# Kernel optimization log

Measured on AMD Instinct MI355X. Metric: run time of the kernel, lower is better.

## Reference

```python
import jax, jax.numpy as jnp
import numpy as np
import math

D_MODEL = 512
KEY_DIM = 128
NUM_LAYERS = 2
TEMP = 30.0
NORM_EPS = 1e-5
NORM_SCALE = math.sqrt(1.0 / (D_MODEL * 4 * 4))


def _l2norm_lastdim(x):
    # F.normalize(x, p=2, dim=-1): x / max(||x||, 1e-12)
    n = jnp.sqrt(jnp.sum(x * x, axis=-1, keepdims=True))
    return x / jnp.maximum(n, 1e-12)


def _attn(q, k, v, WK, bK):
    # q: [Sq,B,D], k: [Sk,B,D], v: [Sk,B,D] -> [Sq,B,D]
    wq = _l2norm_lastdim(q @ WK + bK)            # [Sq,B,K]
    wk = _l2norm_lastdim(k @ WK + bK)            # [Sk,B,K]
    dot = jnp.einsum('qbk,sbk->bqs', wq, wk)     # cosine sims
    aff = jax.nn.softmax(dot * TEMP, axis=-1)
    return jnp.einsum('bqs,sbd->qbd', aff, v)


def _instance_norm(x, h, w):
    # x: [HW,B,D]; InstanceL2Norm over (D,h,w) per batch element, size_average=True
    HW, B, D = x.shape
    ss = jnp.sum(x * x, axis=(0, 2))             # [B]
    factor = NORM_SCALE * jnp.sqrt((D * h * w) / (ss + NORM_EPS))
    return x * factor[None, :, None]


def _encoder(src4d, WKs, bKs):
    B, D, H, W = src4d.shape
    x = src4d.reshape(B, D, H * W).transpose(2, 0, 1)   # [HW,B,D]
    for _ in range(NUM_LAYERS):
        x = _instance_norm(x + _attn(x, x, x, WKs, bKs), H, W)
    return x  # memory [HW,B,D]


def _decoder(tgt4d, memory, pos, WKs, bKs, WKc, bKc):
    B, D, H, W = tgt4d.shape
    x = tgt4d.reshape(B, D, H * W).transpose(2, 0, 1)   # [HW,B,D]
    for _ in range(NUM_LAYERS):
        x = _instance_norm(x + _attn(x, x, x, WKs, bKs), H, W)
        mask = _attn(x, memory, pos, WKc, bKc)
        t2 = _instance_norm(x * mask, H, W)
        t3 = _attn(x, memory, memory * pos, WKc, bKc)
        t4 = _instance_norm(x + t3, H, W)
        x = _instance_norm(t2 + t4, H, W)
    feat = x.reshape(H, W, B, D).transpose(2, 3, 0, 1)  # [B,D,H,W]
    return feat


def setup_inputs() -> dict:
    key = jax.random.key(0)
    k1, k2, k3, k4, k5 = jax.random.split(key, 5)
    B, D, H, W = 16, D_MODEL, 32, 32
    std = math.sqrt(2.0 / KEY_DIM)
    return {
        'train_feat': jax.random.normal(k1, (B, D, H, W), jnp.float32),
        'test_feat': jax.random.normal(k2, (B, D, H, W), jnp.float32),
        'train_label': jax.random.uniform(k3, (B, H, W), jnp.float32),
        'WK_self': jax.random.normal(k4, (D, KEY_DIM), jnp.float32) * std,
        'bK_self': jnp.zeros((KEY_DIM,), jnp.float32),
        'WK_cross': jax.random.normal(k5, (D, KEY_DIM), jnp.float32) * std,
        'bK_cross': jnp.zeros((KEY_DIM,), jnp.float32),
    }


def reference(train_feat, test_feat, train_label, WK_self, bK_self, WK_cross, bK_cross):
    B, D, H, W = train_feat.shape
    memory = _encoder(train_feat, WK_self, bK_self)              # [HW,B,D]
    # pos: label [B,H,W] -> [HW,B,1] -> broadcast to [HW,B,D]
    pos = jnp.broadcast_to(train_label.reshape(B, H * W).T[:, :, None], (H * W, B, D))
    encoded_feat = _decoder(train_feat, memory, pos, WK_self, bK_self, WK_cross, bK_cross)
    decoded_feat = _decoder(test_feat, memory, pos, WK_self, bK_self, WK_cross, bK_cross)
    return (encoded_feat, decoded_feat)
```

## Files before the change

kernel.cpp:

```cpp
#include <hip/hip_runtime.h>
#include <math.h>

#define NB 16
#define SEQ 1024
#define DM 512
#define KD 128
#define TEMP_F 30.0f
#define NS_F 0.011048543456039805f
#define DS_F 524288.0f

#define SS_IDX(grp, b) (((grp) * NB + (b)) * 16)
#define SS_STRIDE 768
#define SS_STAGES 12
#define SS_FLOATS (SS_STRIDE * SS_STAGES)

typedef short bf16x8 __attribute__((ext_vector_type(8)));
typedef float f32x4 __attribute__((ext_vector_type(4)));
typedef unsigned short us;
typedef unsigned short us8 __attribute__((ext_vector_type(8)));

__device__ __forceinline__ us f2bf(float x) {
    union { float f; unsigned u; } v; v.f = x;
    unsigned r = v.u + 0x7fffu + ((v.u >> 16) & 1u);
    return (us)(r >> 16);
}
__device__ __forceinline__ float bf2f(us h) {
    union { unsigned u; float f; } v; v.u = ((unsigned)h) << 16;
    return v.f;
}

#define GLL16(gp, lp) __builtin_amdgcn_global_load_lds( \
    (__attribute__((address_space(1))) void*)(unsigned long long)(gp), \
    (__attribute__((address_space(3))) void*)(unsigned)(unsigned long long)(lp), 16, 0, 0)

__global__ __launch_bounds__(256) void k_transpose_in(const float* __restrict__ src,
                                                      us* __restrict__ XC,
                                                      us* __restrict__ XT) {
    __shared__ float tile[32][33];
    const int b = blockIdx.z;
    const int d0 = blockIdx.x * 32;
    const int s0 = blockIdx.y * 32;
    const int tx = threadIdx.x, ty = threadIdx.y;
    const float* p = src + (size_t)b * DM * SEQ;
    us* pt = XT + (size_t)b * DM * SEQ;
    us* pc = XC + (size_t)b * SEQ * 1024;
#pragma unroll
    for (int j = 0; j < 32; j += 8) {
        const size_t o = (size_t)(d0 + ty + j) * SEQ + s0 + tx;
        const float v = p[o];
        tile[ty + j][tx] = v;
        pt[o] = f2bf(v);
    }
    __syncthreads();
#pragma unroll
    for (int j = 0; j < 4; ++j) {
        const int s = s0 + ty + j * 8;
        const int d = d0 + tx;
        const float v = tile[tx][ty + j * 8];
        const us h = f2bf(v);
        pc[(size_t)s * 1024 + d] = h;
        pc[(size_t)s * 1024 + 512 + d] = f2bf(v - bf2f(h));
    }
}

__global__ __launch_bounds__(256) void k_mklabel(const us* __restrict__ MT,
                                                 const float* __restrict__ label,
                                                 us* __restrict__ ML) {
    const int b = blockIdx.y;
    const size_t off = ((size_t)blockIdx.x * 256 + threadIdx.x) * 8;
    const int s = (int)(off & (SEQ - 1));
    const size_t o = (size_t)b * DM * SEQ + off;
    us8 v = *(const us8*)(MT + o);
    const float4 l0 = *(const float4*)(label + (size_t)b * SEQ + s);
    const float4 l1 = *(const float4*)(label + (size_t)b * SEQ + s + 4);
    us8 r;
    r[0] = f2bf(bf2f(v[0]) * l0.x); r[1] = f2bf(bf2f(v[1]) * l0.y);
    r[2] = f2bf(bf2f(v[2]) * l0.z); r[3] = f2bf(bf2f(v[3]) * l0.w);
    r[4] = f2bf(bf2f(v[4]) * l1.x); r[5] = f2bf(bf2f(v[5]) * l1.y);
    r[6] = f2bf(bf2f(v[6]) * l1.z); r[7] = f2bf(bf2f(v[7]) * l1.w);
    *(us8*)(ML + o) = r;
}

__global__ __launch_bounds__(256) void k_wsplit(const float* __restrict__ WK,
                                                us* __restrict__ WC) {
    const int k = blockIdx.x;
    for (int d = threadIdx.x; d < DM; d += 256) {
        const float v = WK[(size_t)d * KD + k];
        const us h = f2bf(v);
        WC[(size_t)k * 1024 + d] = h;
        WC[(size_t)k * 1024 + 512 + d] = f2bf(v - bf2f(h));
    }
}

__global__ __launch_bounds__(256) void k_proj(const us* __restrict__ XC,
                                              const us* __restrict__ WC,
                                              const float* __restrict__ bK,
                                              us* __restrict__ Wout) {
    const int row0 = blockIdx.x * 32;
    __shared__ short As[32 * 64], Bs[128 * 64];
    __shared__ float ssp[2][32];
    const int tid = threadIdx.x, w = tid >> 6, l = tid & 63;
    const int wm = (w >> 1) * 16, wn = (w & 1) * 64;
    const int sr = l >> 3, sc = (((l & 7) ^ (l >> 3)) << 3);
    const int lr = l & 15, lk = (l >> 4) * 8;
    const int sx = (lr & 7) << 3;
    f32x4 acc[4] = {};
    for (int k0 = 0; k0 < 1536; k0 += 64) {
        const int ak0 = (k0 < 1024) ? k0 : k0 - 1024;
        const int bk0 = (k0 < 512) ? k0 : k0 - 512;
        GLL16(XC + (size_t)(row0 + w * 8 + sr) * 1024 + ak0 + sc, &As[w * 512]);
#pragma unroll
        for (int cc = 0; cc < 4; ++cc) {
            const int c = 4 * w + cc;
            GLL16(WC + (size_t)(c * 8 + sr) * 1024 + bk0 + sc, &Bs[c * 512]);
        }
        __syncthreads();
#pragma unroll
        for (int kc = 0; kc < 2; ++kc) {
            const int kk = kc * 32 + lk;
            const bf16x8 a = *(const bf16x8*)&As[(wm + lr) * 64 + (kk ^ sx)];
            bf16x8 bb[4];
#pragma unroll
            for (int fn = 0; fn < 4; ++fn)
                bb[fn] = *(const bf16x8*)&Bs[(wn + fn * 16 + lr) * 64 + (kk ^ sx)];
#pragma unroll
            for (int fn = 0; fn < 4; ++fn)
                acc[fn] = __builtin_amdgcn_mfma_f32_16x16x32_bf16(a, bb[fn], acc[fn], 0, 0, 0);
        }
        __syncthreads();
    }
    const int er = l & 15, eq = (l >> 4) * 4;
    const int nh = w & 1;
    float bkv[4];
#pragma unroll
    for (int fn = 0; fn < 4; ++fn) bkv[fn] = bK[wn + fn * 16 + er];
    float vv[4][4];
#pragma unroll
    for (int r = 0; r < 4; ++r) {
        float ss = 0.f;
#pragma unroll
        for (int fn = 0; fn < 4; ++fn) {
            const float t = acc[fn][r] + bkv[fn];
            vv[fn][r] = t;
            ss += t * t;
        }
#pragma unroll
        for (int o = 8; o > 0; o >>= 1) ss += __shfl_xor(ss, o, 64);
        if (er == 0) ssp[nh][wm + eq + r] = ss;
    }
    __syncthreads();
#pragma unroll
    for (int r = 0; r < 4; ++r) {
        const int rowloc = wm + eq + r;
        const float tot = ssp[0][rowloc] + ssp[1][rowloc];
        const float invn = 1.0f / fmaxf(sqrtf(tot), 1e-12f);
        const size_t ro = (size_t)(row0 + rowloc) * 256;
#pragma unroll
        for (int fn = 0; fn < 4; ++fn) {
            const float ov = vv[fn][r] * invn;
            const us h = f2bf(ov);
            Wout[ro + wn + fn * 16 + er] = h;
            Wout[ro + 128 + wn + fn * 16 + er] = f2bf(ov - bf2f(h));
        }
    }
}

__global__ __launch_bounds__(512, 2) void k_attn(const us* __restrict__ Qc,
                                                 const us* __restrict__ Kc,
                                                 const us* __restrict__ VT,
                                                 const us* __restrict__ XC,
                                                 const float* __restrict__ labelp,
                                                 float* __restrict__ MVEC,
                                                 float* __restrict__ Cout,
                                                 float* __restrict__ SS, int mode) {
    const int b = blockIdx.x;
    const int q0 = blockIdx.y * 64;
    __shared__ short KL[2][4 * 32 * 64];
    __shared__ short VL[2][512 * 32];
    __shared__ us PL[64 * 40];
    __shared__ float RSL[2][64], RLL[2][64];
    __shared__ float INVL[64], MVL[64];
    __shared__ float LBL[1024];
    __shared__ float ps[3][8];
    const int tid = threadIdx.x, w = tid >> 6, l = tid & 63;
    const int lr = l & 15, g = l >> 4, lk = g * 8;
    const int qa = w & 3, sh = w >> 2;
    const int kx = (lr & 7) << 3;
    const us* Qb = Qc + (size_t)b * SEQ * 256;
    const us* Kb = Kc + (size_t)b * SEQ * 256;
    const us* Vb = VT + (size_t)b * DM * SEQ;

    const us* Qrow = Qb + (size_t)(q0 + qa * 16 + lr) * 256;
    bf16x8 qh[4], ql[4];
#pragma unroll
    for (int kc = 0; kc < 4; ++kc) {
        qh[kc] = *(const bf16x8*)(Qrow + kc * 32 + lk);
        ql[kc] = *(const bf16x8*)(Qrow + 128 + kc * 32 + lk);
    }
#pragma unroll
    for (int i = 0; i < 2; ++i) {
        const int c = w * 2 + i, p = c >> 2, rg = c & 3;
        GLL16(Kb + (size_t)(rg * 8 + (l >> 3)) * 256 + p * 64 + (((l & 7) ^ (l >> 3)) << 3),
              &KL[0][p * 2048 + rg * 512 + l * 8]);
    }
#pragma unroll
    for (int i = 0; i < 4; ++i) {
        const int c = w * 4 + i;
        GLL16(Vb + (size_t)(c * 16 + (l >> 2)) * SEQ + (((l & 3) ^ ((l >> 3) & 3)) << 3),
              &VL[0][c * 512 + l * 8]);
    }
    if (mode == 2 && w < 4)
        GLL16(labelp + (size_t)b * SEQ + w * 256 + l * 4, &LBL[w * 256 + l * 4]);
    __syncthreads();

    f32x4 acc[4][4];
#pragma unroll
    for (int m = 0; m < 4; ++m)
#pragma unroll
        for (int n = 0; n < 4; ++n) acc[m][n] = (f32x4){0.f, 0.f, 0.f, 0.f};
    float rsum[4] = {0.f, 0.f, 0.f, 0.f}, rlsum[4] = {0.f, 0.f, 0.f, 0.f};
    int cur = 0;
    for (int it = 0; it < 32; ++it) {
        const int rowb = (sh * 16 + lr) * 64;
        f32x4 sacc = {};
        bf16x8 kf[4];
#pragma unroll
        for (int kc = 0; kc < 4; ++kc)
            kf[kc] = *(const bf16x8*)&KL[cur][(kc >> 1) * 2048 + rowb + ((((kc & 1) << 5) + lk) ^ kx)];
        __builtin_amdgcn_s_setprio(1);
#pragma unroll
        for (int kc = 0; kc < 4; ++kc)
            sacc = __builtin_amdgcn_mfma_f32_16x16x32_bf16(qh[kc], kf[kc], sacc, 0, 0, 0);
#pragma unroll
        for (int kc = 0; kc < 4; ++kc)
            sacc = __builtin_amdgcn_mfma_f32_16x16x32_bf16(ql[kc], kf[kc], sacc, 0, 0, 0);
        __builtin_amdgcn_s_setprio(0);
#pragma unroll
        for (int kc = 0; kc < 4; ++kc)
            kf[kc] = *(const bf16x8*)&KL[cur][(2 + (kc >> 1)) * 2048 + rowb + ((((kc & 1) << 5) + lk) ^ kx)];
        __builtin_amdgcn_s_setprio(1);
#pragma unroll
        for (int kc = 0; kc < 4; ++kc)
            sacc = __builtin_amdgcn_mfma_f32_16x16x32_bf16(qh[kc], kf[kc], sacc, 0, 0, 0);
        __builtin_amdgcn_s_setprio(0);
        const float lb = (mode == 2) ? LBL[it * 32 + sh * 16 + lr] : 0.f;
#pragma unroll
        for (int r = 0; r < 4; ++r) {
            const float e = __expf(fmaf(TEMP_F, sacc[r], -TEMP_F));
            rsum[r] += e;
            rlsum[r] += e * lb;
            PL[(qa * 16 + g * 4 + r) * 40 + sh * 16 + lr] = f2bf(e);
        }
        __syncthreads();
        if (it < 31) {
            const int s1 = (it + 1) * 32, nb2 = cur ^ 1;
#pragma unroll
            for (int i = 0; i < 2; ++i) {
                const int c = w * 2 + i, p = c >> 2, rg = c & 3;
                GLL16(Kb + (size_t)(s1 + rg * 8 + (l >> 3)) * 256 + p * 64 + (((l & 7) ^ (l >> 3)) << 3),
                      &KL[nb2][p * 2048 + rg * 512 + l * 8]);
            }
#pragma unroll
            for (int i = 0; i < 4; ++i) {
                const int c = w * 4 + i;
                GLL16(Vb + (size_t)(c * 16 + (l >> 2)) * SEQ + s1 + (((l & 3) ^ ((l >> 3) & 3)) << 3),
                      &VL[nb2][c * 512 + l * 8]);
            }
        }
        bf16x8 pa[4], vb[4];
#pragma unroll
        for (int m = 0; m < 4; ++m)
            pa[m] = *(const bf16x8*)&PL[(m * 16 + lr) * 40 + lk];
#pragma unroll
        for (int n = 0; n < 4; ++n) {
            const int d = w * 64 + n * 16 + lr;
            vb[n] = *(const bf16x8*)&VL[cur][d * 32 + ((g ^ ((d >> 1) & 3)) << 3)];
        }
        __builtin_amdgcn_s_setprio(1);
#pragma unroll
        for (int m = 0; m < 4; ++m)
#pragma unroll
            for (int n = 0; n < 4; ++n)
                acc[m][n] = __builtin_amdgcn_mfma_f32_16x16x32_bf16(pa[m], vb[n], acc[m][n], 0, 0, 0);
        __builtin_amdgcn_s_setprio(0);
        __syncthreads();
        cur ^= 1;
    }

#pragma unroll
    for (int o = 1; o < 16; o <<= 1)
#pragma unroll
        for (int r = 0; r < 4; ++r) {
            rsum[r] += __shfl_xor(rsum[r], o, 64);
            rlsum[r] += __shfl_xor(rlsum[r], o, 64);
        }
    if (lr == 0) {
#pragma unroll
        for (int r = 0; r < 4; ++r) {
            RSL[sh][qa * 16 + g * 4 + r] = rsum[r];
            RLL[sh][qa * 16 + g * 4 + r] = rlsum[r];
        }
    }
    __syncthreads();
    if (tid < 64) {
        const float tot = RSL[0][tid] + RSL[1][tid];
        const float iv = 1.0f / tot;
        INVL[tid] = iv;
        const float mvv = (RLL[0][tid] + RLL[1][tid]) * iv;
        MVL[tid] = mvv;
        if (mode == 2) MVEC[(size_t)b * SEQ + q0 + tid] = mvv;
    }
    __syncthreads();

    const us* XCb = XC + (size_t)b * SEQ * 1024;
    float sa = 0.f, sb = 0.f, sab = 0.f;
#pragma unroll
    for (int m = 0; m < 4; ++m)
#pragma unroll
        for (int r = 0; r < 4; ++r) {
            const int q = m * 16 + g * 4 + r;
            const float iv = INVL[q];
            const float mvq = MVL[q];
            const int row = q0 + q;
#pragma unroll
            for (int n = 0; n < 4; ++n) {
                const int col = w * 64 + n * 16 + lr;
                float v = acc[m][n][r] * iv;
                const size_t o = ((size_t)b * SEQ + row) * DM + col;
                const size_t xo = (size_t)row * 1024 + col;
                const float x = bf2f(XCb[xo]) + bf2f(XCb[xo + 512]);
                v += x;
                sb += v * v;
                if (mode == 2) { const float a = x * mvq; sa += a * a; sab += a * v; }
                Cout[o] = v;
            }
        }
#pragma unroll
    for (int off = 32; off > 0; off >>= 1) {
        sb += __shfl_xor(sb, off, 64);
        if (mode == 2) { sa += __shfl_xor(sa, off, 64); sab += __shfl_xor(sab, off, 64); }
    }
    if (l == 0) { ps[0][w] = sb; ps[1][w] = sa; ps[2][w] = sab; }
    __syncthreads();
    if (tid == 0) {
        float t0 = 0.f, t1 = 0.f, t2 = 0.f;
#pragma unroll
        for (int i = 0; i < 8; ++i) { t0 += ps[0][i]; t1 += ps[1][i]; t2 += ps[2][i]; }
        if (mode == 1) {
            atomicAdd(&SS[SS_IDX(0, b)], t0);
        } else {
            atomicAdd(&SS[SS_IDX(0, b)], t1);
            atomicAdd(&SS[SS_IDX(1, b)], t0);
            atomicAdd(&SS[SS_IDX(2, b)], t2);
        }
    }
}

__global__ void k_zero(float* __restrict__ SSb) {
    const int i = blockIdx.x * 256 + threadIdx.x;
    if (i < SS_FLOATS) SSb[i] = 0.0f;
}

__global__ __launch_bounds__(256) void k_finish(const float* __restrict__ Tin,
                                                const us* __restrict__ XCin,
                                                const float* __restrict__ mv,
                                                const float* __restrict__ SS,
                                                us* __restrict__ XCout,
                                                us* __restrict__ XTb,
                                                float* __restrict__ XTf,
                                                int mode, int writeXC) {
    const int b = blockIdx.z;
    const int s0 = blockIdx.x * 32, d0 = blockIdx.y * 32;
    const int tx = threadIdx.x, ty = threadIdx.y;
    __shared__ float tile[32][33];
    float f1 = 0.f, f2 = 0.f, f3;
    if (mode == 0) {
        f3 = NS_F * sqrtf(DS_F / (SS[SS_IDX(0, b)] + 1e-5f));
    } else {
        const float ssa = SS[SS_IDX(0, b)], ssb = SS[SS_IDX(1, b)], ssab = SS[SS_IDX(2, b)];
        f1 = NS_F * sqrtf(DS_F / (ssa + 1e-5f));
        f2 = NS_F * sqrtf(DS_F / (ssb + 1e-5f));
        const float ssc = f1 * f1 * ssa + 2.f * f1 * f2 * ssab + f2 * f2 * ssb;
        f3 = NS_F * sqrtf(DS_F / (ssc + 1e-5f));
    }
#pragma unroll
    for (int j = 0; j < 4; ++j) {
        const int s = s0 + ty + j * 8;
        const int d = d0 + tx;
        const size_t o = ((size_t)b * SEQ + s) * DM + d;
        const size_t xo = ((size_t)b * SEQ + s) * 1024 + d;
        float v;
        if (mode == 0) v = f3 * Tin[o];
        else {
            const float x = bf2f(XCin[xo]) + bf2f(XCin[xo + 512]);
            v = f3 * (f1 * x * mv[(size_t)b * SEQ + s] + f2 * Tin[o]);
        }
        if (writeXC) {
            const us h = f2bf(v);
            XCout[xo] = h;
            XCout[xo + 512] = f2bf(v - bf2f(h));
        }
        tile[ty + j * 8][tx] = v;
    }
    __syncthreads();
#pragma unroll
    for (int j = 0; j < 4; ++j) {
        const int d = d0 + ty + j * 8;
        const int s = s0 + tx;
        const float v = tile[tx][ty + j * 8];
        const size_t o = ((size_t)b * DM + d) * SEQ + s;
        if (XTb) XTb[o] = f2bf(v);
        else if (XTf) XTf[o] = v;
    }
}

extern "C" void kernel_launch(void* const* d_in, const int* in_sizes, int n_in,
                              void* d_out, int out_size, void* d_ws, size_t ws_size,
                              hipStream_t stream) {
    const float* train_feat = (const float*)d_in[0];
    const float* test_feat  = (const float*)d_in[1];
    const float* label      = (const float*)d_in[2];
    const float* WKs        = (const float*)d_in[3];
    const float* bKs        = (const float*)d_in[4];
    const float* WKc        = (const float*)d_in[5];
    const float* bKc        = (const float*)d_in[6];
    float* out = (float*)d_out;
    float* w = (float*)d_ws;

    const size_t SBD = (size_t)NB * SEQ * DM;
    const size_t SBK = (size_t)NB * SEQ * KD;

    float* T   = w;
    us* XC     = (us*)(T + SBD);
    us* XTd    = XC + 2 * SBD;
    us* MEMT   = XTd + SBD;
    us* MEMLT  = MEMT + SBD;
    us* W1C    = MEMLT + SBD;
    us* WKMC   = W1C + 2 * SBK;
    us* WCs    = WKMC + 2 * SBK;
    us* WCc    = WCs + (size_t)KD * 1024;
    float* MVEC = (float*)(WCc + (size_t)KD * 1024);
    float* SS   = MVEC + (size_t)NB * SEQ;

    const dim3 gT_in(DM / 32, SEQ / 32, NB), bT(32, 8);
    const dim3 gFin(SEQ / 32, DM / 32, NB);
    const dim3 gAtt(NB, SEQ / 64);

    int stage = 0;
    auto nextSS = [&]() { return SS + (size_t)(stage++) * SS_STRIDE; };

    k_zero<<<(SS_FLOATS + 255) / 256, 256, 0, stream>>>(SS);
    k_wsplit<<<KD, 256, 0, stream>>>(WKs, WCs);
    k_wsplit<<<KD, 256, 0, stream>>>(WKc, WCc);

    k_transpose_in<<<gT_in, bT, 0, stream>>>(train_feat, XC, MEMT);
    for (int l = 0; l < 2; ++l) {
        float* SSst = nextSS();
        k_proj<<<NB * SEQ / 32, 256, 0, stream>>>(XC, WCs, bKs, W1C);
        k_attn<<<gAtt, 512, 0, stream>>>(W1C, W1C, MEMT, XC, nullptr, nullptr, T, SSst, 1);
        k_finish<<<gFin, bT, 0, stream>>>(T, XC, nullptr, SSst, XC, MEMT, nullptr, 0, 1);
    }
    k_proj<<<NB * SEQ / 32, 256, 0, stream>>>(XC, WCc, bKc, WKMC);
    k_mklabel<<<dim3(DM * SEQ / 8 / 256, NB), 256, 0, stream>>>(MEMT, label, MEMLT);

    auto decoder = [&](const float* feat, float* outp) {
        k_transpose_in<<<gT_in, bT, 0, stream>>>(feat, XC, XTd);
        for (int l = 0; l < 2; ++l) {
            float* SSst = nextSS();
            k_proj<<<NB * SEQ / 32, 256, 0, stream>>>(XC, WCs, bKs, W1C);
            k_attn<<<gAtt, 512, 0, stream>>>(W1C, W1C, XTd, XC, nullptr, nullptr, T, SSst, 1);
            k_finish<<<gFin, bT, 0, stream>>>(T, XC, nullptr, SSst, XC, XTd, nullptr, 0, 1);
            float* SSst2 = nextSS();
            k_proj<<<NB * SEQ / 32, 256, 0, stream>>>(XC, WCc, bKc, W1C);
            k_attn<<<gAtt, 512, 0, stream>>>(W1C, WKMC, MEMLT, XC, label, MVEC, T, SSst2, 2);
            if (l == 0)
                k_finish<<<gFin, bT, 0, stream>>>(T, XC, MVEC, SSst2, XC, XTd, nullptr, 1, 1);
            else
                k_finish<<<gFin, bT, 0, stream>>>(T, XC, MVEC, SSst2, XC, nullptr, outp, 1, 0);
        }
    };
    decoder(train_feat, out);
    decoder(test_feat, out + SBD);
}
```

Measured before the change: 984.3 us.

## Shrink attention tile to 32 queries and read V directly from global

The attention kernel now handles 32 query rows per block with 4 waves instead of 64 rows with 8 waves, doubling the grid. It drops the shared-memory V staging and double buffer, and each wave loads its V fragments straight from global memory every iteration while covering 128 output columns. This cuts LDS use and the async V copies, but each block re-reads V for fewer queries, roughly doubling global V traffic. It also loses the latency hiding that the prefetched V buffer gave.

```diff
diff --git a/kernel.cpp b/kernel.cpp
--- a/kernel.cpp
+++ b/kernel.cpp
@@ -165,7 +165,7 @@
     }
 }
 
-__global__ __launch_bounds__(512, 2) void k_attn(const us* __restrict__ Qc,
+__global__ __launch_bounds__(256, 2) void k_attn(const us* __restrict__ Qc,
                                                  const us* __restrict__ Kc,
                                                  const us* __restrict__ VT,
                                                  const us* __restrict__ XC,
@@ -174,17 +174,16 @@
                                                  float* __restrict__ Cout,
                                                  float* __restrict__ SS, int mode) {
     const int b = blockIdx.x;
-    const int q0 = blockIdx.y * 64;
+    const int q0 = blockIdx.y * 32;
     __shared__ short KL[2][4 * 32 * 64];
-    __shared__ short VL[2][512 * 32];
-    __shared__ us PL[64 * 40];
-    __shared__ float RSL[2][64], RLL[2][64];
-    __shared__ float INVL[64], MVL[64];
+    __shared__ us PL[32 * 40];
+    __shared__ float RSL[2][32], RLL[2][32];
+    __shared__ float INVL[32], MVL[32];
     __shared__ float LBL[1024];
-    __shared__ float ps[3][8];
+    __shared__ float ps[3][4];
     const int tid = threadIdx.x, w = tid >> 6, l = tid & 63;
     const int lr = l & 15, g = l >> 4, lk = g * 8;
-    const int qa = w & 3, sh = w >> 2;
+    const int qa = w & 1, sh = w >> 1;
     const int kx = (lr & 7) << 3;
     const us* Qb = Qc + (size_t)b * SEQ * 256;
     const us* Kb = Kc + (size_t)b * SEQ * 256;
@@ -198,29 +197,28 @@
         ql[kc] = *(const bf16x8*)(Qrow + 128 + kc * 32 + lk);
     }
 #pragma unroll
-    for (int i = 0; i < 2; ++i) {
-        const int c = w * 2 + i, p = c >> 2, rg = c & 3;
+    for (int i = 0; i < 4; ++i) {
+        const int c = w * 4 + i, p = c >> 2, rg = c & 3;
         GLL16(Kb + (size_t)(rg * 8 + (l >> 3)) * 256 + p * 64 + (((l & 7) ^ (l >> 3)) << 3),
               &KL[0][p * 2048 + rg * 512 + l * 8]);
     }
-#pragma unroll
-    for (int i = 0; i < 4; ++i) {
-        const int c = w * 4 + i;
-        GLL16(Vb + (size_t)(c * 16 + (l >> 2)) * SEQ + (((l & 3) ^ ((l >> 3) & 3)) << 3),
-              &VL[0][c * 512 + l * 8]);
-    }
-    if (mode == 2 && w < 4)
+    if (mode == 2)
         GLL16(labelp + (size_t)b * SEQ + w * 256 + l * 4, &LBL[w * 256 + l * 4]);
     __syncthreads();
 
-    f32x4 acc[4][4];
-#pragma unroll
-    for (int m = 0; m < 4; ++m)
-#pragma unroll
-        for (int n = 0; n < 4; ++n) acc[m][n] = (f32x4){0.f, 0.f, 0.f, 0.f};
+    f32x4 acc[2][8];
+#pragma unroll
+    for (int m = 0; m < 2; ++m)
+#pragma unroll
+        for (int n = 0; n < 8; ++n) acc[m][n] = (f32x4){0.f, 0.f, 0.f, 0.f};
     float rsum[4] = {0.f, 0.f, 0.f, 0.f}, rlsum[4] = {0.f, 0.f, 0.f, 0.f};
     int cur = 0;
     for (int it = 0; it < 32; ++it) {
+        const int s0 = it * 32;
+        bf16x8 vb[8];
+#pragma unroll
+        for (int n = 0; n < 8; ++n)
+            vb[n] = *(const bf16x8*)(Vb + (size_t)(w * 128 + n * 16 + lr) * 1024 + s0 + lk);
         const int rowb = (sh * 16 + lr) * 64;
         f32x4 sacc = {};
         bf16x8 kf[4];
@@ -243,7 +241,7 @@
         for (int kc = 0; kc < 4; ++kc)
             sacc = __builtin_amdgcn_mfma_f32_16x16x32_bf16(qh[kc], kf[kc], sacc, 0, 0, 0);
         __builtin_amdgcn_s_setprio(0);
-        const float lb = (mode == 2) ? LBL[it * 32 + sh * 16 + lr] : 0.f;
+        const float lb = (mode == 2) ? LBL[s0 + sh * 16 + lr] : 0.f;
 #pragma unroll
         for (int r = 0; r < 4; ++r) {
             const float e = __expf(fmaf(TEMP_F, sacc[r], -TEMP_F));
@@ -253,34 +251,22 @@
         }
         __syncthreads();
         if (it < 31) {
-            const int s1 = (it + 1) * 32, nb2 = cur ^ 1;
-#pragma unroll
-            for (int i = 0; i < 2; ++i) {
-                const int c = w * 2 + i, p = c >> 2, rg = c & 3;
+            const int s1 = s0 + 32, nb2 = cur ^ 1;
+#pragma unroll
+            for (int i = 0; i < 4; ++i) {
+                const int c = w * 4 + i, p = c >> 2, rg = c & 3;
                 GLL16(Kb + (size_t)(s1 + rg * 8 + (l >> 3)) * 256 + p * 64 + (((l & 7) ^ (l >> 3)) << 3),
                       &KL[nb2][p * 2048 + rg * 512 + l * 8]);
             }
-#pragma unroll
-            for (int i = 0; i < 4; ++i) {
-                const int c = w * 4 + i;
-                GLL16(Vb + (size_t)(c * 16 + (l >> 2)) * SEQ + s1 + (((l & 3) ^ ((l >> 3) & 3)) << 3),
-                      &VL[nb2][c * 512 + l * 8]);
-            }
-        }
-        bf16x8 pa[4], vb[4];
-#pragma unroll
-        for (int m = 0; m < 4; ++m)
-            pa[m] = *(const bf16x8*)&PL[(m * 16 + lr) * 40 + lk];
-#pragma unroll
-        for (int n = 0; n < 4; ++n) {
-            const int d = w * 64 + n * 16 + lr;
-            vb[n] = *(const bf16x8*)&VL[cur][d * 32 + ((g ^ ((d >> 1) & 3)) << 3)];
-        }
+        }
+        bf16x8 pa[2];
+        pa[0] = *(const bf16x8*)&PL[lr * 40 + lk];
+        pa[1] = *(const bf16x8*)&PL[(16 + lr) * 40 + lk];
         __builtin_amdgcn_s_setprio(1);
 #pragma unroll
-        for (int m = 0; m < 4; ++m)
-#pragma unroll
-            for (int n = 0; n < 4; ++n)
+        for (int m = 0; m < 2; ++m)
+#pragma unroll
+            for (int n = 0; n < 8; ++n)
                 acc[m][n] = __builtin_amdgcn_mfma_f32_16x16x32_bf16(pa[m], vb[n], acc[m][n], 0, 0, 0);
         __builtin_amdgcn_s_setprio(0);
         __syncthreads();
@@ -302,7 +288,7 @@
         }
     }
     __syncthreads();
-    if (tid < 64) {
+    if (tid < 32) {
         const float tot = RSL[0][tid] + RSL[1][tid];
         const float iv = 1.0f / tot;
         INVL[tid] = iv;
@@ -315,7 +301,7 @@
     const us* XCb = XC + (size_t)b * SEQ * 1024;
     float sa = 0.f, sb = 0.f, sab = 0.f;
 #pragma unroll
-    for (int m = 0; m < 4; ++m)
+    for (int m = 0; m < 2; ++m)
 #pragma unroll
         for (int r = 0; r < 4; ++r) {
             const int q = m * 16 + g * 4 + r;
@@ -323,8 +309,8 @@
             const float mvq = MVL[q];
             const int row = q0 + q;
 #pragma unroll
-            for (int n = 0; n < 4; ++n) {
-                const int col = w * 64 + n * 16 + lr;
+            for (int n = 0; n < 8; ++n) {
+                const int col = w * 128 + n * 16 + lr;
                 float v = acc[m][n][r] * iv;
                 const size_t o = ((size_t)b * SEQ + row) * DM + col;
                 const size_t xo = (size_t)row * 1024 + col;
@@ -345,7 +331,7 @@
     if (tid == 0) {
         float t0 = 0.f, t1 = 0.f, t2 = 0.f;
 #pragma unroll
-        for (int i = 0; i < 8; ++i) { t0 += ps[0][i]; t1 += ps[1][i]; t2 += ps[2][i]; }
+        for (int i = 0; i < 4; ++i) { t0 += ps[0][i]; t1 += ps[1][i]; t2 += ps[2][i]; }
         if (mode == 1) {
             atomicAdd(&SS[SS_IDX(0, b)], t0);
         } else {
@@ -444,7 +430,7 @@
 
     const dim3 gT_in(DM / 32, SEQ / 32, NB), bT(32, 8);
     const dim3 gFin(SEQ / 32, DM / 32, NB);
-    const dim3 gAtt(NB, SEQ / 64);
+    const dim3 gAtt(NB, SEQ / 32);
 
     int stage = 0;
     auto nextSS = [&]() { return SS + (size_t)(stage++) * SS_STRIDE; };
@@ -457,7 +443,7 @@
     for (int l = 0; l < 2; ++l) {
         float* SSst = nextSS();
         k_proj<<<NB * SEQ / 32, 256, 0, stream>>>(XC, WCs, bKs, W1C);
-        k_attn<<<gAtt, 512, 0, stream>>>(W1C, W1C, MEMT, XC, nullptr, nullptr, T, SSst, 1);
+        k_attn<<<gAtt, 256, 0, stream>>>(W1C, W1C, MEMT, XC, nullptr, nullptr, T, SSst, 1);
         k_finish<<<gFin, bT, 0, stream>>>(T, XC, nullptr, SSst, XC, MEMT, nullptr, 0, 1);
     }
     k_proj<<<NB * SEQ / 32, 256, 0, stream>>>(XC, WCc, bKc, WKMC);
@@ -468,11 +454,11 @@
         for (int l = 0; l < 2; ++l) {
             float* SSst = nextSS();
             k_proj<<<NB * SEQ / 32, 256, 0, stream>>>(XC, WCs, bKs, W1C);
-            k_attn<<<gAtt, 512, 0, stream>>>(W1C, W1C, XTd, XC, nullptr, nullptr, T, SSst, 1);
+            k_attn<<<gAtt, 256, 0, stream>>>(W1C, W1C, XTd, XC, nullptr, nullptr, T, SSst, 1);
             k_finish<<<gFin, bT, 0, stream>>>(T, XC, nullptr, SSst, XC, XTd, nullptr, 0, 1);
             float* SSst2 = nextSS();
             k_proj<<<NB * SEQ / 32, 256, 0, stream>>>(XC, WCc, bKc, W1C);
-            k_attn<<<gAtt, 512, 0, stream>>>(W1C, WKMC, MEMLT, XC, label, MVEC, T, SSst2, 2);
+            k_attn<<<gAtt, 256, 0, stream>>>(W1C, WKMC, MEMLT, XC, label, MVEC, T, SSst2, 2);
             if (l == 0)
                 k_finish<<<gFin, bT, 0, stream>>>(T, XC, MVEC, SSst2, XC, XTd, nullptr, 1, 1);
             else
```

After: 1.274 ms. 1.29x slower.

## Load V fragments directly from global and transpose score MFMA for vectorized P writes

Applied to the files above, without the earlier changes.

The V tile is no longer staged through double-buffered LDS. Each wave now reads its bf16 V fragments straight from global memory every iteration, which frees a large block of shared memory and drops the LDS write/read traffic. The score MFMA operands are swapped so each lane holds one query row and four key columns. This lets the P tile be written with a single 4-element vector store, the labels be read as a float4, and the row sums be reduced with only two shuffles. The cost is global-load latency on the critical path of every iteration, with no prefetch, and possible L2 pressure from the repeated V reads.

```diff
diff --git a/kernel.cpp b/kernel.cpp
--- a/kernel.cpp
+++ b/kernel.cpp
@@ -17,6 +17,7 @@
 typedef short bf16x8 __attribute__((ext_vector_type(8)));
 typedef float f32x4 __attribute__((ext_vector_type(4)));
 typedef unsigned short us;
+typedef unsigned short us4v __attribute__((ext_vector_type(4)));
 typedef unsigned short us8 __attribute__((ext_vector_type(8)));
 
 __device__ __forceinline__ us f2bf(float x) {
@@ -176,7 +177,6 @@
     const int b = blockIdx.x;
     const int q0 = blockIdx.y * 64;
     __shared__ short KL[2][4 * 32 * 64];
-    __shared__ short VL[2][512 * 32];
     __shared__ us PL[64 * 40];
     __shared__ float RSL[2][64], RLL[2][64];
     __shared__ float INVL[64], MVL[64];
@@ -203,12 +203,6 @@
         GLL16(Kb + (size_t)(rg * 8 + (l >> 3)) * 256 + p * 64 + (((l & 7) ^ (l >> 3)) << 3),
               &KL[0][p * 2048 + rg * 512 + l * 8]);
     }
-#pragma unroll
-    for (int i = 0; i < 4; ++i) {
-        const int c = w * 4 + i;
-        GLL16(Vb + (size_t)(c * 16 + (l >> 2)) * SEQ + (((l & 3) ^ ((l >> 3) & 3)) << 3),
-              &VL[0][c * 512 + l * 8]);
-    }
     if (mode == 2 && w < 4)
         GLL16(labelp + (size_t)b * SEQ + w * 256 + l * 4, &LBL[w * 256 + l * 4]);
     __syncthreads();
@@ -218,9 +212,14 @@
     for (int m = 0; m < 4; ++m)
 #pragma unroll
         for (int n = 0; n < 4; ++n) acc[m][n] = (f32x4){0.f, 0.f, 0.f, 0.f};
-    float rsum[4] = {0.f, 0.f, 0.f, 0.f}, rlsum[4] = {0.f, 0.f, 0.f, 0.f};
+    float rs = 0.f, rl = 0.f;
     int cur = 0;
     for (int it = 0; it < 32; ++it) {
+        const int s0 = it * 32;
+        bf16x8 vb[4];
+#pragma unroll
+        for (int n = 0; n < 4; ++n)
+            vb[n] = *(const bf16x8*)(Vb + (size_t)(w * 64 + n * 16 + lr) * 1024 + s0 + lk);
         const int rowb = (sh * 16 + lr) * 64;
         f32x4 sacc = {};
         bf16x8 kf[4];
@@ -230,10 +229,10 @@
         __builtin_amdgcn_s_setprio(1);
 #pragma unroll
         for (int kc = 0; kc < 4; ++kc)
-            sacc = __builtin_amdgcn_mfma_f32_16x16x32_bf16(qh[kc], kf[kc], sacc, 0, 0, 0);
+            sacc = __builtin_amdgcn_mfma_f32_16x16x32_bf16(kf[kc], qh[kc], sacc, 0, 0, 0);
 #pragma unroll
         for (int kc = 0; kc < 4; ++kc)
-            sacc = __builtin_amdgcn_mfma_f32_16x16x32_bf16(ql[kc], kf[kc], sacc, 0, 0, 0);
+            sacc = __builtin_amdgcn_mfma_f32_16x16x32_bf16(kf[kc], ql[kc], sacc, 0, 0, 0);
         __builtin_amdgcn_s_setprio(0);
 #pragma unroll
         for (int kc = 0; kc < 4; ++kc)
@@ -241,41 +240,37 @@
         __builtin_amdgcn_s_setprio(1);
 #pragma unroll
         for (int kc = 0; kc < 4; ++kc)
-            sacc = __builtin_amdgcn_mfma_f32_16x16x32_bf16(qh[kc], kf[kc], sacc, 0, 0, 0);
+            sacc = __builtin_amdgcn_mfma_f32_16x16x32_bf16(kf[kc], qh[kc], sacc, 0, 0, 0);
         __builtin_amdgcn_s_setprio(0);
-        const float lb = (mode == 2) ? LBL[it * 32 + sh * 16 + lr] : 0.f;
+        const int sbase = sh * 16 + g * 4;
+        float lb4[4] = {0.f, 0.f, 0.f, 0.f};
+        if (mode == 2) {
+            const float4 t = *(const float4*)&LBL[s0 + sbase];
+            lb4[0] = t.x; lb4[1] = t.y; lb4[2] = t.z; lb4[3] = t.w;
+        }
+        us4v pw;
 #pragma unroll
         for (int r = 0; r < 4; ++r) {
             const float e = __expf(fmaf(TEMP_F, sacc[r], -TEMP_F));
-            rsum[r] += e;
-            rlsum[r] += e * lb;
-            PL[(qa * 16 + g * 4 + r) * 40 + sh * 16 + lr] = f2bf(e);
-        }
+            rs += e;
+            rl += e * lb4[r];
+            pw[r] = f2bf(e);
+        }
+        *(us4v*)&PL[(qa * 16 + lr) * 40 + sbase] = pw;
         __syncthreads();
         if (it < 31) {
-            const int s1 = (it + 1) * 32, nb2 = cur ^ 1;
+            const int s1 = s0 + 32, nb2 = cur ^ 1;
 #pragma unroll
             for (int i = 0; i < 2; ++i) {
                 const int c = w * 2 + i, p = c >> 2, rg = c & 3;
                 GLL16(Kb + (size_t)(s1 + rg * 8 + (l >> 3)) * 256 + p * 64 + (((l & 7) ^ (l >> 3)) << 3),
                       &KL[nb2][p * 2048 + rg * 512 + l * 8]);
             }
-#pragma unroll
-            for (int i = 0; i < 4; ++i) {
-                const int c = w * 4 + i;
-                GLL16(Vb + (size_t)(c * 16 + (l >> 2)) * SEQ + s1 + (((l & 3) ^ ((l >> 3) & 3)) << 3),
-                      &VL[nb2][c * 512 + l * 8]);
-            }
-        }
-        bf16x8 pa[4], vb[4];
+        }
+        bf16x8 pa[4];
 #pragma unroll
         for (int m = 0; m < 4; ++m)
             pa[m] = *(const bf16x8*)&PL[(m * 16 + lr) * 40 + lk];
-#pragma unroll
-        for (int n = 0; n < 4; ++n) {
-            const int d = w * 64 + n * 16 + lr;
-            vb[n] = *(const bf16x8*)&VL[cur][d * 32 + ((g ^ ((d >> 1) & 3)) << 3)];
-        }
         __builtin_amdgcn_s_setprio(1);
 #pragma unroll
         for (int m = 0; m < 4; ++m)
@@ -287,19 +282,13 @@
         cur ^= 1;
     }
 
-#pragma unroll
-    for (int o = 1; o < 16; o <<= 1)
-#pragma unroll
-        for (int r = 0; r < 4; ++r) {
-            rsum[r] += __shfl_xor(rsum[r], o, 64);
-            rlsum[r] += __shfl_xor(rlsum[r], o, 64);
-        }
-    if (lr == 0) {
-#pragma unroll
-        for (int r = 0; r < 4; ++r) {
-            RSL[sh][qa * 16 + g * 4 + r] = rsum[r];
-            RLL[sh][qa * 16 + g * 4 + r] = rlsum[r];
-        }
+    rs += __shfl_xor(rs, 16, 64);
+    rs += __shfl_xor(rs, 32, 64);
+    rl += __shfl_xor(rl, 16, 64);
+    rl += __shfl_xor(rl, 32, 64);
+    if (g == 0) {
+        RSL[sh][qa * 16 + lr] = rs;
+        RLL[sh][qa * 16 + lr] = rl;
     }
     __syncthreads();
     if (tid < 64) {
```

Result: slower. 1.028 ms (+4.4%).
